# Kernel optimization log

Hardware: AMD Instinct MI355X
Metric: run time of the kernel (lower is better)

Reference implementation:

```python
import jax, jax.numpy as jnp
import numpy as np

B, L, M, D = 8, 2048, 2048, 256


def setup_inputs() -> dict:
    key = jax.random.key(0)
    k1, k2, k3, k4, k5 = jax.random.split(key, 5)
    inp = jax.random.normal(k1, (B, L, D), dtype=jnp.float32)
    mem = jax.random.normal(k2, (B, M, D), dtype=jnp.float32)
    mask = jnp.ones((B, M), dtype=jnp.float32)
    # Learned parameters (Linear(D, 1, bias=False) -> weight vector of shape [D])
    w_input = jax.random.normal(k3, (D,), dtype=jnp.float32) / np.sqrt(D)
    w_memory = jax.random.normal(k4, (D,), dtype=jnp.float32) / np.sqrt(D)
    dot_scale = jax.random.uniform(k5, (D,), dtype=jnp.float32, minval=0.0, maxval=1.0 / np.sqrt(D))
    return {"input": inp, "memory": mem, "mask": mask,
            "w_input": w_input, "w_memory": w_memory, "dot_scale": dot_scale}


def reference(input, memory, mask, w_input, w_memory, dot_scale):
    # dropout with p=0.0 / eval mode -> identity
    input_dot = jnp.einsum('bld,d->bl', input, w_input)[:, :, None]      # [B, L, 1]
    memory_dot = jnp.einsum('bmd,d->bm', memory, w_memory)[:, None, :]   # [B, 1, M]
    cross_dot = jnp.einsum('bld,bmd->blm', input * dot_scale, memory)    # [B, L, M]
    att = input_dot + memory_dot + cross_dot                             # [B, L, M]
    att = att - 1e30 * (1.0 - mask[:, None, :])
    weight_one = jax.nn.softmax(att, axis=-1)                            # [B, L, M]
    output_one = jnp.einsum('blm,bmd->bld', weight_one, memory)          # [B, L, D]
    weight_two = jax.nn.softmax(jnp.max(att, axis=-1), axis=-1)[:, None, :]  # [B, 1, L]
    output_two = jnp.einsum('bol,bld->bod', weight_two, input)           # [B, 1, D]
    return jnp.concatenate(
        [input, output_one, input * output_one, output_two * output_one], axis=-1)
```

## Files before the change

### kernel.cpp

```cpp
#include <hip/hip_runtime.h>
#include <hip/hip_bf16.h>


typedef __bf16 bf16_t;
typedef bf16_t bf16x4 __attribute__((ext_vector_type(4)));
typedef bf16_t bf16x8 __attribute__((ext_vector_type(8)));
typedef float  f32x16 __attribute__((ext_vector_type(16)));
typedef unsigned int u32x2 __attribute__((ext_vector_type(2)));
typedef unsigned int u32x4 __attribute__((ext_vector_type(4)));

#define NB 8
#define NL 2048
#define NM 2048
#define ND 256
#define OUTW 1024
#define MT 64
#define MH 1024
#define NIT 16
#define LT 128
#define MEMT_X0 8388608u
#define FLASH_LDS 163840

__device__ __forceinline__ unsigned omap(unsigned x) {
    return ((x >> 10) << 12) | (x & 1023u);
}

__device__ __forceinline__ void dma16(const void* g, void* l) {
    __builtin_amdgcn_global_load_lds(
        (const __attribute__((address_space(1))) unsigned int*)g,
        (__attribute__((address_space(3))) unsigned int*)l, 16, 0, 0);
}

__global__ __launch_bounds__(256) void prep_kernel(
    const float* __restrict__ memory, const float* __restrict__ mask,
    const float* __restrict__ w_memory,
    float* __restrict__ ws_mbias, float* __restrict__ ws_numden,
    char* __restrict__ outc)
{
    __shared__ __align__(16) bf16_t lds[32 * 264];

    int b  = blockIdx.x >> 6;
    int mc = blockIdx.x & 63;
    int t  = threadIdx.x, w = t >> 6, lane = t & 63;

    if (blockIdx.x == 0) {
        for (int k = t; k < 2056; k += 256) ws_numden[k] = 0.f;
    }

    float4 wv = *(const float4*)(w_memory + lane * 4);

    #pragma unroll
    for (int it = 0; it < 8; ++it) {
        int rloc = it * 4 + w;
        int row  = b * NM + mc * 32 + rloc;
        float4 v = *(const float4*)(memory + (size_t)row * ND + lane * 4);
        float s = v.x * wv.x + v.y * wv.y + v.z * wv.z + v.w * wv.w;
        #pragma unroll
        for (int off = 1; off < 64; off <<= 1) s += __shfl_xor(s, off, 64);
        if (lane == 0) ws_mbias[row] = s - 1e30f * (1.0f - mask[row]);
        bf16x4 bv;
        bv[0] = (bf16_t)v.x; bv[1] = (bf16_t)v.y;
        bv[2] = (bf16_t)v.z; bv[3] = (bf16_t)v.w;
        *(bf16x4*)(&lds[rloc * 264 + lane * 4]) = bv;
    }
    __syncthreads();

    {
        unsigned xbase = ((unsigned)(b * 64 + mc)) * 16384u;
        int c = t & 31, h5 = (t >> 5) & 1, ksh = t >> 6;
        #pragma unroll
        for (int r = 0; r < 4; ++r) {
            bf16x8 g = *(const bf16x8*)(&lds[c * 264 + (4 * r + ksh) * 16 + h5 * 8]);
            *(bf16x8*)(outc + omap(xbase + r * 4096u + (unsigned)t * 16u)) = g;
        }
    }

    int d = t;
    #pragma unroll
    for (int mc4 = 0; mc4 < 4; ++mc4) {
        bf16x8 pk;
        #pragma unroll
        for (int j = 0; j < 8; ++j) pk[j] = lds[(mc4 * 8 + j) * 264 + d];
        unsigned x = MEMT_X0 +
            2u * ((((unsigned)(b * 256 + mc * 4 + mc4)) * ND + d) * 8);
        *(bf16x8*)(outc + omap(x)) = pk;
    }
}

__global__ __launch_bounds__(512, 2) void flash_kernel(
    const float* __restrict__ input, const float* __restrict__ dot_scale,
    const float* __restrict__ w_input, const float* __restrict__ ws_mbias,
    const char* __restrict__ outc, float* __restrict__ out,
    float* __restrict__ ws_l, float* __restrict__ ws_m,
    float* __restrict__ ws_idot)
{
    extern __shared__ __align__(16) char smem[];

    int bid = blockIdx.x;
    int half = bid & 1, b = (bid >> 1) & 7, lt = bid >> 4;
    int l0 = lt * LT;
    int m_base = half * MH;
    int t = threadIdx.x, w = t >> 6, lane = t & 63;
    int gw = w & 3, grp = w >> 2;
    int c = lane & 31, h = lane >> 5;

    const float* qrow = input + (size_t)(b * NL + l0 + gw * 32 + c) * ND;
    bool do_idot = (half == 0) && (grp == 0);
    float idot_s = 0.f;
    bf16x8 qf[16];
    #pragma unroll
    for (int ks = 0; ks < 16; ++ks) {
        int d0 = ks * 16 + h * 8;
        float4 a0 = *(const float4*)(qrow + d0);
        float4 a1 = *(const float4*)(qrow + d0 + 4);
        float4 s0 = *(const float4*)(dot_scale + d0);
        float4 s1 = *(const float4*)(dot_scale + d0 + 4);
        if (do_idot) {
            float4 w0 = *(const float4*)(w_input + d0);
            float4 w1 = *(const float4*)(w_input + d0 + 4);
            idot_s += a0.x * w0.x + a0.y * w0.y + a0.z * w0.z + a0.w * w0.w
                    + a1.x * w1.x + a1.y * w1.y + a1.z * w1.z + a1.w * w1.w;
        }
        qf[ks][0] = (bf16_t)(a0.x * s0.x); qf[ks][1] = (bf16_t)(a0.y * s0.y);
        qf[ks][2] = (bf16_t)(a0.z * s0.z); qf[ks][3] = (bf16_t)(a0.w * s0.w);
        qf[ks][4] = (bf16_t)(a1.x * s1.x); qf[ks][5] = (bf16_t)(a1.y * s1.y);
        qf[ks][6] = (bf16_t)(a1.z * s1.z); qf[ks][7] = (bf16_t)(a1.w * s1.w);
    }
    if (do_idot) {
        idot_s += __shfl_xor(idot_s, 32, 64);
        if (lane < 32) ws_idot[b * NL + l0 + gw * 32 + lane] = idot_s;
    }

    unsigned xk = ((unsigned)(b * 64 + half * 32 + grp)) * 16384u + (unsigned)lane * 16u;
    const char* kg = outc + omap(xk);
    unsigned xv = MEMT_X0 +
        2u * ((((unsigned)(b * 256 + (m_base >> 3) + grp * 4 + h)) * ND + c) * 8);
    const char* vg = outc + omap(xv);

    char* kbase = smem;
    char* vbase = smem + 98304;

    #define STAGE_K(nbuf) do {                                                \
        _Pragma("unroll")                                                     \
        for (int j = 0; j < 4; ++j) {                                         \
            int i = gw * 4 + j;                                               \
            dma16(kg + i * 4096, (nbuf) + grp * 16384 + i * 1024);            \
        }                                                                     \
        kg += 131072; } while (0)

    #define STAGE_V(nbuf) do {                                                \
        _Pragma("unroll")                                                     \
        for (int j = 0; j < 4; ++j) {                                         \
            int i = gw * 4 + j;                                               \
            int ks = i >> 3, dt = i & 7;                                      \
            dma16(vg + ks * 32768 + (dt >> 1) * 4096 + (dt & 1) * 512,        \
                  (nbuf) + grp * 16384 + i * 1024);                           \
        }                                                                     \
        vg += 131072; } while (0)

    STAGE_K(kbase);
    asm volatile("" ::: "memory");
    STAGE_V(vbase);
    asm volatile("" ::: "memory");
    STAGE_K(kbase + 32768);
    asm volatile("" ::: "memory");

    f32x16 oaccT[8];
    #pragma unroll
    for (int i = 0; i < 8; ++i)
        #pragma unroll
        for (int r = 0; r < 16; ++r) oaccT[i][r] = 0.f;
    float lsum = 0.f, mmax = -3e38f;

    const float* mb_base = ws_mbias + b * NM;

    unsigned kcur = 0, kst = 65536;
    unsigned vcur = 0, vst = 32768;

    #pragma unroll 1
    for (int it = 0; it < NIT; ++it) {
        int m0 = m_base + it * MT + grp * 32;
        asm volatile("s_waitcnt vmcnt(4)" ::: "memory");
        if (it == NIT - 1) asm volatile("s_waitcnt vmcnt(0)" ::: "memory");
        __syncthreads();
        const bf16_t* kb = (const bf16_t*)(kbase + kcur + grp * 16384);
        const bf16_t* vb = (const bf16_t*)(vbase + vcur + grp * 16384);
        const float* mrow = mb_base + m0 + 4 * h;
        float4 mbv0 = *(const float4*)(mrow);
        float4 mbv1 = *(const float4*)(mrow + 8);
        float4 mbv2 = *(const float4*)(mrow + 16);
        float4 mbv3 = *(const float4*)(mrow + 24);
        asm volatile("" ::: "memory");
        if (it + 1 < NIT) { STAGE_V(vbase + vst); }
        asm volatile("" ::: "memory");
        if (it + 2 < NIT) { STAGE_K(kbase + kst); }
        asm volatile("" ::: "memory");
        f32x16 S;
        #pragma unroll
        for (int r = 0; r < 16; ++r) S[r] = 0.f;
        #pragma unroll
        for (int ks = 0; ks < 16; ++ks) {
            bf16x8 k0 = *(const bf16x8*)(kb + ks * 512 + lane * 8);
            S = __builtin_amdgcn_mfma_f32_32x32x16_bf16(k0, qf[ks], S, 0, 0, 0);
        }
        u32x2 own[4];
        #pragma unroll
        for (int g = 0; g < 4; ++g) {
            float4 mbv = (g == 0) ? mbv0 : (g == 1) ? mbv1 : (g == 2) ? mbv2 : mbv3;
            bf16x4 tq;
            #pragma unroll
            for (int q = 0; q < 4; ++q) {
                float v = S[g * 4 + q] +
                          ((q == 0) ? mbv.x : (q == 1) ? mbv.y : (q == 2) ? mbv.z : mbv.w);
                mmax = fmaxf(mmax, v);
                float e = __expf(v);
                lsum += e;
                tq[q] = (bf16_t)e;
            }
            own[g] = __builtin_bit_cast(u32x2, tq);
        }
        #pragma unroll
        for (int ks = 0; ks < 2; ++ks) {
            unsigned oAlo = own[2 * ks].x,     oAhi = own[2 * ks].y;
            unsigned oBlo = own[2 * ks + 1].x, oBhi = own[2 * ks + 1].y;
            unsigned slo = h ? oAlo : oBlo;
            unsigned shi = h ? oAhi : oBhi;
            unsigned rlo = (unsigned)__shfl_xor((int)slo, 32, 64);
            unsigned rhi = (unsigned)__shfl_xor((int)shi, 32, 64);
            unsigned mlo = h ? oBlo : oAlo;
            unsigned mhi = h ? oBhi : oAhi;
            u32x4 uu;
            uu.x = h ? rlo : mlo;
            uu.y = h ? rhi : mhi;
            uu.z = h ? mlo : rlo;
            uu.w = h ? mhi : rhi;
            bf16x8 pb = __builtin_bit_cast(bf16x8, uu);
            #pragma unroll
            for (int dt = 0; dt < 8; ++dt) {
                bf16x8 vv = *(const bf16x8*)(vb + (ks * 8 + dt) * 512 + lane * 8);
                oaccT[dt] = __builtin_amdgcn_mfma_f32_32x32x16_bf16(vv, pb, oaccT[dt], 0, 0, 0);
            }
        }
        kcur = (kcur == 65536u) ? 0u : kcur + 32768u;
        kst  = (kst  == 65536u) ? 0u : kst + 32768u;
        vcur ^= 32768u; vst ^= 32768u;
    }
    #undef STAGE_K
    #undef STAGE_V

    __syncthreads();
    if (grp == 1) {
        float* dst = (float*)(smem + gw * 32768);
        #pragma unroll
        for (int dt = 0; dt < 8; ++dt) {
            #pragma unroll
            for (int q = 0; q < 4; ++q) {
                float4 v4;
                v4.x = oaccT[dt][q * 4 + 0]; v4.y = oaccT[dt][q * 4 + 1];
                v4.z = oaccT[dt][q * 4 + 2]; v4.w = oaccT[dt][q * 4 + 3];
                *(float4*)(dst + dt * 1024 + q * 256 + lane * 4) = v4;
            }
        }
        float* aux = (float*)(smem + 131072 + gw * 512);
        aux[lane] = lsum;
        aux[64 + lane] = mmax;
    }
    __syncthreads();
    if (grp == 0) {
        const float* src = (const float*)(smem + gw * 32768);
        #pragma unroll
        for (int dt = 0; dt < 8; ++dt) {
            #pragma unroll
            for (int q = 0; q < 4; ++q) {
                float4 v4 = *(const float4*)(src + dt * 1024 + q * 256 + lane * 4);
                oaccT[dt][q * 4 + 0] += v4.x; oaccT[dt][q * 4 + 1] += v4.y;
                oaccT[dt][q * 4 + 2] += v4.z; oaccT[dt][q * 4 + 3] += v4.w;
            }
        }
        const float* aux = (const float*)(smem + 131072 + gw * 512);
        lsum += aux[lane];
        mmax = fmaxf(mmax, aux[64 + lane]);
    }
    __syncthreads();
    if (grp == 0) {
        mmax = fmaxf(mmax, __shfl_xor(mmax, 32, 64));
        lsum += __shfl_xor(lsum, 32, 64);
        if (lane < 32) {
            int row = b * NL + l0 + gw * 32 + lane;
            ws_l[half * (NB * NL) + row] = lsum;
            ws_m[half * (NB * NL) + row] = mmax;
        }
        float* patch = (float*)(smem + gw * 4352);
        float* oseg = out + (size_t)(b * NL + l0 + gw * 32) * OUTW + ND * (1 + half);
        #pragma unroll
        for (int dt = 0; dt < 8; ++dt) {
            asm volatile("s_waitcnt lgkmcnt(0)" ::: "memory");
            #pragma unroll
            for (int r = 0; r < 16; ++r)
                patch[((r & 3) + 8 * (r >> 2) + 4 * h) * 33 + c] = oaccT[dt][r];
            asm volatile("s_waitcnt lgkmcnt(0)" ::: "memory");
            #pragma unroll
            for (int rr = 0; rr < 16; ++rr) {
                float val = patch[c * 33 + rr * 2 + h];
                oseg[(size_t)(rr * 2 + h) * OUTW + dt * 32 + c] = val;
            }
        }
    }
}

__global__ __launch_bounds__(256) void o2_kernel(
    const float* __restrict__ input, const float* __restrict__ ws_idot,
    const float* __restrict__ ws_m, float* __restrict__ ws_num,
    float* __restrict__ ws_den)
{
    __shared__ float4 red[256];
    int b = blockIdx.x >> 5, slice = blockIdx.x & 31;
    int t = threadIdx.x;
    int lgrp = t >> 6, d4 = (t & 63) * 4;
    float4 acc = {0.f, 0.f, 0.f, 0.f};
    float esum = 0.f;
    for (int i = 0; i < 16; ++i) {
        int row = b * NL + slice * 64 + lgrp * 16 + i;
        float e = __expf(ws_idot[row] + fmaxf(ws_m[row], ws_m[NB * NL + row]));
        float4 v = *(const float4*)(input + (size_t)row * ND + d4);
        acc.x += e * v.x; acc.y += e * v.y;
        acc.z += e * v.z; acc.w += e * v.w;
        esum += e;
    }
    red[t] = acc;
    __syncthreads();
    if (t < 64) {
        float4 a0 = red[t], a1 = red[t + 64], a2 = red[t + 128], a3 = red[t + 192];
        float* dst = ws_num + b * ND + t * 4;
        atomicAdd(dst + 0, a0.x + a1.x + a2.x + a3.x);
        atomicAdd(dst + 1, a0.y + a1.y + a2.y + a3.y);
        atomicAdd(dst + 2, a0.z + a1.z + a2.z + a3.z);
        atomicAdd(dst + 3, a0.w + a1.w + a2.w + a3.w);
    }
    if ((t & 63) == 0) atomicAdd(ws_den + b, esum);
}

__global__ __launch_bounds__(256) void assembly_kernel(
    const float* __restrict__ input, const float* __restrict__ ws_num,
    const float* __restrict__ ws_den, const float* __restrict__ ws_l,
    float* __restrict__ out)
{
    size_t tid = (size_t)blockIdx.x * 256 + threadIdx.x;
    size_t row = tid >> 6;
    int d = (int)(tid & 63) * 4;
    int b = (int)(row >> 11);
    float inv  = 1.0f / (ws_l[row] + ws_l[NB * NL + row]);
    float dinv = 1.0f / ws_den[b];
    float* po = out + row * OUTW;
    float4 in = *(const float4*)(input + row * ND + d);
    float4 pa = *(const float4*)(po + ND + d);
    float4 pb = *(const float4*)(po + 2 * ND + d);
    float4 nu = *(const float4*)(ws_num + b * ND + d);
    float4 o1;
    o1.x = (pa.x + pb.x) * inv; o1.y = (pa.y + pb.y) * inv;
    o1.z = (pa.z + pb.z) * inv; o1.w = (pa.w + pb.w) * inv;
    float4 o2v;
    o2v.x = nu.x * dinv; o2v.y = nu.y * dinv;
    o2v.z = nu.z * dinv; o2v.w = nu.w * dinv;
    *(float4*)(po + d) = in;
    *(float4*)(po + ND + d) = o1;
    float4 q;
    q.x = in.x * o1.x; q.y = in.y * o1.y; q.z = in.z * o1.z; q.w = in.w * o1.w;
    *(float4*)(po + 2 * ND + d) = q;
    float4 r;
    r.x = o2v.x * o1.x; r.y = o2v.y * o1.y; r.z = o2v.z * o1.z; r.w = o2v.w * o1.w;
    *(float4*)(po + 3 * ND + d) = r;
}

extern "C" void kernel_launch(void* const* d_in, const int* in_sizes, int n_in,
                              void* d_out, int out_size, void* d_ws, size_t ws_size,
                              hipStream_t stream) {
    const float* input     = (const float*)d_in[0];
    const float* memory    = (const float*)d_in[1];
    const float* mask      = (const float*)d_in[2];
    const float* w_input   = (const float*)d_in[3];
    const float* w_memory  = (const float*)d_in[4];
    const float* dot_scale = (const float*)d_in[5];
    float* out = (float*)d_out;
    char* outc = (char*)d_out;
    float* ws  = (float*)d_ws;

    float* ws_idot  = ws;
    float* ws_mbias = ws + 16384;
    float* ws_l     = ws + 32768;
    float* ws_m     = ws + 65536;
    float* ws_num   = ws + 98304;
    float* ws_den   = ws + 100352;

    prep_kernel<<<512, 256, 0, stream>>>(memory, mask, w_memory, ws_mbias,
                                         ws_num, outc);
    flash_kernel<<<256, 512, FLASH_LDS, stream>>>(input, dot_scale, w_input,
                                                  ws_mbias, outc, out,
                                                  ws_l, ws_m, ws_idot);
    o2_kernel<<<256, 256, 0, stream>>>(input, ws_idot, ws_m, ws_num, ws_den);
    assembly_kernel<<<4096, 256, 0, stream>>>(input, ws_num, ws_den, ws_l, out);
}
```

Baseline: 196.6 us.

## Software-pipeline QK^T MFMA one tile ahead of softmax and PV

Restructures the flash-attention main loop so the QK^T score MFMAs for the next memory tile are issued after the current tile's softmax, overlapping them with the PV MFMAs and exp work. The prologue computes the first tile's scores before the loop. The wait for DMA loads moves from a partial vmcnt(4) at the top of each iteration to a full vmcnt(0) plus barrier at the end. This raises instruction-level overlap between the matrix and vector units, but the full wait may expose more global-load latency, and the extra live score registers add pressure.

```diff
diff --git a/kernel.cpp b/kernel.cpp
--- a/kernel.cpp
+++ b/kernel.cpp
@@ -159,11 +159,8 @@
         vg += 131072; } while (0)
 
     STAGE_K(kbase);
-    asm volatile("" ::: "memory");
     STAGE_V(vbase);
-    asm volatile("" ::: "memory");
     STAGE_K(kbase + 32768);
-    asm volatile("" ::: "memory");
 
     f32x16 oaccT[8];
     #pragma unroll
@@ -174,35 +171,36 @@
 
     const float* mb_base = ws_mbias + b * NM;
 
-    unsigned kcur = 0, kst = 65536;
-    unsigned vcur = 0, vst = 32768;
+    asm volatile("s_waitcnt vmcnt(0)" ::: "memory");
+    __syncthreads();
+
+    f32x16 S;
+    #pragma unroll
+    for (int r = 0; r < 16; ++r) S[r] = 0.f;
+    {
+        const bf16_t* kb = (const bf16_t*)(kbase + grp * 16384);
+        #pragma unroll
+        for (int ks = 0; ks < 16; ++ks) {
+            bf16x8 k0 = *(const bf16x8*)(kb + ks * 512 + lane * 8);
+            S = __builtin_amdgcn_mfma_f32_32x32x16_bf16(k0, qf[ks], S, 0, 0, 0);
+        }
+    }
+
+    unsigned kq  = 32768u;
+    unsigned kst = 65536u;
+    unsigned vpv = 0u;
+    unsigned vst = 32768u;
 
     #pragma unroll 1
     for (int it = 0; it < NIT; ++it) {
         int m0 = m_base + it * MT + grp * 32;
-        asm volatile("s_waitcnt vmcnt(4)" ::: "memory");
-        if (it == NIT - 1) asm volatile("s_waitcnt vmcnt(0)" ::: "memory");
-        __syncthreads();
-        const bf16_t* kb = (const bf16_t*)(kbase + kcur + grp * 16384);
-        const bf16_t* vb = (const bf16_t*)(vbase + vcur + grp * 16384);
+        if (it + 1 < NIT) { STAGE_V(vbase + vst); }
+        if (it + 2 < NIT) { STAGE_K(kbase + kst); }
         const float* mrow = mb_base + m0 + 4 * h;
         float4 mbv0 = *(const float4*)(mrow);
         float4 mbv1 = *(const float4*)(mrow + 8);
         float4 mbv2 = *(const float4*)(mrow + 16);
         float4 mbv3 = *(const float4*)(mrow + 24);
-        asm volatile("" ::: "memory");
-        if (it + 1 < NIT) { STAGE_V(vbase + vst); }
-        asm volatile("" ::: "memory");
-        if (it + 2 < NIT) { STAGE_K(kbase + kst); }
-        asm volatile("" ::: "memory");
-        f32x16 S;
-        #pragma unroll
-        for (int r = 0; r < 16; ++r) S[r] = 0.f;
-        #pragma unroll
-        for (int ks = 0; ks < 16; ++ks) {
-            bf16x8 k0 = *(const bf16x8*)(kb + ks * 512 + lane * 8);
-            S = __builtin_amdgcn_mfma_f32_32x32x16_bf16(k0, qf[ks], S, 0, 0, 0);
-        }
         u32x2 own[4];
         #pragma unroll
         for (int g = 0; g < 4; ++g) {
@@ -219,6 +217,17 @@
             }
             own[g] = __builtin_bit_cast(u32x2, tq);
         }
+        if (it + 1 < NIT) {
+            const bf16_t* kb = (const bf16_t*)(kbase + kq + grp * 16384);
+            #pragma unroll
+            for (int r = 0; r < 16; ++r) S[r] = 0.f;
+            #pragma unroll
+            for (int ks = 0; ks < 16; ++ks) {
+                bf16x8 k0 = *(const bf16x8*)(kb + ks * 512 + lane * 8);
+                S = __builtin_amdgcn_mfma_f32_32x32x16_bf16(k0, qf[ks], S, 0, 0, 0);
+            }
+        }
+        const bf16_t* vb = (const bf16_t*)(vbase + vpv + grp * 16384);
         #pragma unroll
         for (int ks = 0; ks < 2; ++ks) {
             unsigned oAlo = own[2 * ks].x,     oAhi = own[2 * ks].y;
@@ -241,14 +250,15 @@
                 oaccT[dt] = __builtin_amdgcn_mfma_f32_32x32x16_bf16(vv, pb, oaccT[dt], 0, 0, 0);
             }
         }
-        kcur = (kcur == 65536u) ? 0u : kcur + 32768u;
-        kst  = (kst  == 65536u) ? 0u : kst + 32768u;
-        vcur ^= 32768u; vst ^= 32768u;
+        asm volatile("s_waitcnt vmcnt(0)" ::: "memory");
+        __syncthreads();
+        kq  = (kq  == 65536u) ? 0u : kq  + 32768u;
+        kst = (kst == 65536u) ? 0u : kst + 32768u;
+        vpv ^= 32768u; vst ^= 32768u;
     }
     #undef STAGE_K
     #undef STAGE_V
 
-    __syncthreads();
     if (grp == 1) {
         float* dst = (float*)(smem + gw * 32768);
         #pragma unroll
```

After: 212.3 us. +8.0%, slower.
